# Performance work log

Measured on AMD Instinct MI355X. Metric: run time of the kernel, lower is better.

The kernel has to match this reference:

```python
import jax, jax.numpy as jnp
import numpy as np

KH = KW = 3
STRIDE = 1
PAD = 1
DIL = 1


def _bilinear_gather(data, py, px):
    # data: [B,C,H,W]; py,px: [B,KK,Ho,Wo] absolute sample coords
    B, C, H, W = data.shape
    y0 = jnp.floor(py)
    x0 = jnp.floor(px)
    wy1 = py - y0  # frac weights
    wx1 = px - x0
    wy0 = 1.0 - wy1
    wx0 = 1.0 - wx1
    flat = data.reshape(B, C, H * W)

    def gather(yi, xi):
        valid = (yi >= 0) & (yi < H) & (xi >= 0) & (xi < W)
        yc = jnp.clip(yi, 0, H - 1).astype(jnp.int32)
        xc = jnp.clip(xi, 0, W - 1).astype(jnp.int32)
        idx = yc * W + xc  # [B,KK,Ho,Wo]
        vals = jax.vmap(lambda im, ix: im[:, ix])(flat, idx)  # [B,C,KK,Ho,Wo]
        return vals * valid[:, None].astype(data.dtype)

    out = (gather(y0, x0) * (wy0 * wx0)[:, None]
           + gather(y0, x0 + 1) * (wy0 * wx1)[:, None]
           + gather(y0 + 1, x0) * (wy1 * wx0)[:, None]
           + gather(y0 + 1, x0 + 1) * (wy1 * wx1)[:, None])
    return out  # [B,C,KK,Ho,Wo]


def setup_inputs() -> dict:
    key = jax.random.key(0)
    k1, k2, k3 = jax.random.split(key, 3)
    data = jax.random.normal(k1, (8, 64, 128, 128), dtype=jnp.float32)
    offset = jax.random.normal(k2, (8, 18, 128, 128), dtype=jnp.float32)
    n = 64 * KH * KW
    stdv = 1.0 / np.sqrt(n)
    weight = jax.random.uniform(k3, (64, 64, KH, KW), dtype=jnp.float32,
                                minval=-stdv, maxval=stdv)
    return {"data": data, "offset": offset, "weight": weight}


def reference(data, offset, weight):
    B, C, H, W = data.shape
    Ho = (H + 2 * PAD - (DIL * (KH - 1) + 1)) // STRIDE + 1
    Wo = (W + 2 * PAD - (DIL * (KW - 1) + 1)) // STRIDE + 1
    KK = KH * KW
    # offset layout (deformable_groups=1): [B, 2*KK, Ho, Wo], interleaved (dy, dx) per kernel pt
    off = offset.reshape(B, KK, 2, Ho, Wo)
    off_y = off[:, :, 0]  # [B,KK,Ho,Wo]
    off_x = off[:, :, 1]
    ki = (jnp.arange(KK) // KW).astype(data.dtype)  # kernel row
    kj = (jnp.arange(KK) % KW).astype(data.dtype)   # kernel col
    base_y = (jnp.arange(Ho, dtype=data.dtype) * STRIDE - PAD)[None, :, None] \
             + (ki * DIL)[:, None, None]            # [KK,Ho,1]
    base_x = (jnp.arange(Wo, dtype=data.dtype) * STRIDE - PAD)[None, None, :] \
             + (kj * DIL)[:, None, None]            # [KK,1,Wo]
    py = off_y + base_y[None]  # [B,KK,Ho,Wo]
    px = off_x + base_x[None]
    sampled = _bilinear_gather(data, py, px)  # [B,C,KK,Ho,Wo]
    O = weight.shape[0]
    out = jnp.einsum('bckhw,ock->bohw', sampled, weight.reshape(O, C, KK))
    return out
```

## Files before the change

kernel.cpp:

```cpp
#include <hip/hip_runtime.h>

#define HH 128
#define WW 128
#define CC 64
#define OO 64
#define KK 9
#define PLANE (HH * WW)

#define BAND 11
#define PXB 72
#define BAND_B (BAND * 128 * PXB)
#define POOL_SLOTS 64
#define POOL_OFF BAND_B
#define POOL_B (POOL_SLOTS * 144)
#define DESC_OFF (POOL_OFF + POOL_B)
#define LDS_TOTAL (DESC_OFF + KK * 256 * 16)

typedef _Float16 half8v __attribute__((ext_vector_type(8)));
typedef _Float16 half2v __attribute__((ext_vector_type(2)));
typedef float floatx4 __attribute__((ext_vector_type(4)));

__device__ __forceinline__ unsigned pkpair(float a, float b) {
    return __builtin_bit_cast(unsigned, __builtin_amdgcn_cvt_pkrtz(a, b));
}
__device__ __forceinline__ half2v h2(unsigned u) {
    return __builtin_bit_cast(half2v, u);
}

__global__ __launch_bounds__(256)
void prep_kernel(const float* __restrict__ in, const float* __restrict__ wsrc,
                 unsigned short* __restrict__ outT, _Float16* __restrict__ wt4) {
    __shared__ unsigned tile[64 * 36];
    int blk = blockIdx.x;
    int t = threadIdx.x;
    if (blk < 2048) {
        int b = blk & 7;
        int rest = blk >> 3;
        int y = rest >> 1;
        int xh = rest & 1;
        int p = t & 63;
        int cg = t >> 6;
        const float* src = in + (size_t)(b * 64) * PLANE + y * WW + xh * 64 + p;
#pragma unroll
        for (int i = 0; i < 8; ++i) {
            int c0 = cg * 16 + 2 * i;
            float v0 = src[(size_t)c0 * PLANE];
            float v1 = src[(size_t)(c0 + 1) * PLANE];
            unsigned lo = __builtin_bit_cast(unsigned short, (_Float16)v0);
            unsigned hi = __builtin_bit_cast(unsigned short, (_Float16)v1);
            tile[p * 36 + (c0 >> 1)] = lo | (hi << 16);
        }
        __syncthreads();
        int p2 = t >> 2;
        int q = t & 3;
        const unsigned* s = &tile[p2 * 36 + q * 8];
        uint4 w0 = *(const uint4*)s;
        uint4 w1 = *(const uint4*)(s + 4);
        int half = q >> 1;
        char* dst = (char*)outT + ((size_t)(b * 2 + half) << 20)
                  + (size_t)(y * 128 + xh * 64 + p2) * 64 + (q & 1) * 32;
        *(uint4*)dst = w0;
        *(uint4*)(dst + 16) = w1;
    } else {
        int idx = (blk - 2048) * 256 + t;
        if (idx < 2 * KK * 4 * 64 * 8) {
            int j = idx & 7;
            int lane = (idx >> 3) & 63;
            int nt = (idx >> 9) & 3;
            int pk = idx >> 11;
            int k = pk % 9;
            int pass = pk / 9;
            int o = nt * 16 + (lane & 15);
            int c = pass * 32 + (lane >> 4) * 8 + j;
            wt4[idx] = (_Float16)wsrc[(o * 64 + c) * 9 + k];
        }
    }
}

__global__ __launch_bounds__(1024, 4)
void deform_mfma_kernel(const unsigned short* __restrict__ dataT,
                        const float* __restrict__ offset,
                        const _Float16* __restrict__ wt4,
                        float* __restrict__ out) {
    __shared__ __align__(16) char SB[LDS_TOTAL];
    __shared__ unsigned ovfSrc[POOL_SLOTS];
    __shared__ int ovfCnt;

    const int t = threadIdx.x;
    const int lane = t & 63;
    const int w = t >> 6;
    const int quad = lane >> 4;
    const int l15 = lane & 15;
    const int raw = blockIdx.x;
    const int b = raw & 7;
    const int ho0 = (raw >> 3) * 2;
    const int bs = min(max(ho0 - 4, 0), HH - BAND);

    if (t == 0) ovfCnt = 0;
    __syncthreads();

#pragma unroll
    for (int i = 0; i < 3; ++i) {
        int u = i * 1024 + t;
        if (u < KK * 256) {
            int p = u & 255;
            int k = u >> 8;
            int x = p & 127;
            int ho = ho0 + (p >> 7);
            const float* offp = offset + ((size_t)(b * 18) + 2 * k) * PLANE + ho * WW + x;
            float oy = offp[0];
            float ox = offp[PLANE];
            float py = (float)(ho - 1 + k / 3) + oy;
            float pxx = (float)(x - 1 + k % 3) + ox;
            float y0f = floorf(py);
            float x0f = floorf(pxx);
            float fy = py - y0f;
            float fx = pxx - x0f;
            int y0 = (int)y0f, x0 = (int)x0f;
            int y1 = y0 + 1, x1 = x0 + 1;
            float wy0 = (1.f - fy) * ((y0 >= 0 && y0 < HH) ? 1.f : 0.f);
            float wy1 = fy * ((y1 >= 0 && y1 < HH) ? 1.f : 0.f);
            float wx0 = (1.f - fx) * ((x0 >= 0 && x0 < WW) ? 1.f : 0.f);
            float wx1 = fx * ((x1 >= 0 && x1 < WW) ? 1.f : 0.f);
            int yc0 = min(max(y0, 0), HH - 1);
            int yc1 = min(max(y1, 0), HH - 1);
            int x_lo = min(max(x0, 0), WW - 2);
            float wA = ((x0 == x_lo) ? wx0 : 0.f) + ((x1 == x_lo) ? wx1 : 0.f);
            float wB = ((x0 == x_lo + 1) ? wx0 : 0.f) + ((x1 == x_lo + 1) ? wx1 : 0.f);

            unsigned off0, off1;
            {
                int r = yc0 - bs;
                if (wy0 == 0.f) off0 = (unsigned)(x_lo * PXB);
                else if ((unsigned)r < BAND) off0 = (unsigned)((r * 128 + x_lo) * PXB);
                else {
                    int slot = atomicAdd(&ovfCnt, 1);
                    if (slot < POOL_SLOTS) {
                        ovfSrc[slot] = (unsigned)((yc0 * 128 + x_lo) * 64);
                        off0 = (unsigned)(POOL_OFF + slot * 144);
                    } else {
                        int rc = min(max(r, 0), BAND - 1);
                        off0 = (unsigned)((rc * 128 + x_lo) * PXB);
                    }
                }
            }
            {
                int r = yc1 - bs;
                if (wy1 == 0.f) off1 = (unsigned)(x_lo * PXB);
                else if ((unsigned)r < BAND) off1 = (unsigned)((r * 128 + x_lo) * PXB);
                else {
                    int slot = atomicAdd(&ovfCnt, 1);
                    if (slot < POOL_SLOTS) {
                        ovfSrc[slot] = (unsigned)((yc1 * 128 + x_lo) * 64);
                        off1 = (unsigned)(POOL_OFF + slot * 144);
                    } else {
                        int rc = min(max(r, 0), BAND - 1);
                        off1 = (unsigned)((rc * 128 + x_lo) * PXB);
                    }
                }
            }
            uint4 d;
            d.x = (off0 >> 3) | ((off1 >> 3) << 16);
            d.y = pkpair(wy0 * wA, wy0 * wB);
            d.z = pkpair(wy1 * wA, wy1 * wB);
            d.w = 0;
            *(uint4*)(SB + DESC_OFF + (size_t)(k * 256 + p) * 16) = d;
        }
    }
    __syncthreads();
    const int cnt = min(ovfCnt, POOL_SLOTS);

    floatx4 acc[4];
#pragma unroll
    for (int nt = 0; nt < 4; ++nt)
        acc[nt] = (floatx4){0.f, 0.f, 0.f, 0.f};

    const unsigned qoff = (unsigned)(quad * 16);

    for (int pass = 0; pass < 2; ++pass) {
        if (pass) __syncthreads();
        const char* gh = (const char*)dataT + ((size_t)(b * 2 + pass) << 20);
        {
            const char* gsrc = gh + (unsigned)(bs * 8192);
#pragma unroll
            for (int i = 0; i < 5; ++i) {
                int u = i * 1024 + t;
                uint4 v = *(const uint4*)(gsrc + (size_t)u * 16);
                int pxl = u >> 2, q = u & 3;
                *(uint4*)(SB + pxl * PXB + q * 16) = v;
            }
            if (t < 512) {
                int u = 5120 + t;
                uint4 v = *(const uint4*)(gsrc + (size_t)u * 16);
                int pxl = u >> 2, q = u & 3;
                *(uint4*)(SB + pxl * PXB + q * 16) = v;
            }
            if (t < cnt * 8) {
                int s = t >> 3, j = t & 7, ps = j >> 2, q = j & 3;
                uint4 v = *(const uint4*)(gh + ovfSrc[s] + ps * 64 + q * 16);
                *(uint4*)(SB + POOL_OFF + s * 144 + ps * 72 + q * 16) = v;
            }
        }
        __syncthreads();

        for (int k = 0; k < KK; ++k) {
            uint4 bfr[4];
            const uint4* wk = (const uint4*)wt4 + (size_t)((pass * 9 + k) * 4) * 64 + lane;
#pragma unroll
            for (int nt = 0; nt < 4; ++nt) bfr[nt] = wk[nt * 64];

            int p = w * 16 + l15;
            uint4 d = *(const uint4*)(SB + DESC_OFF + (size_t)(k * 256 + p) * 16);
            unsigned off0 = (d.x & 0xffffu) << 3;
            unsigned off1 = (d.x >> 16) << 3;
            half2v wv0 = h2(d.y), wv1 = h2(d.z);
            half2v h00 = __builtin_shufflevector(wv0, wv0, 0, 0);
            half2v h01 = __builtin_shufflevector(wv0, wv0, 1, 1);
            half2v h10 = __builtin_shufflevector(wv1, wv1, 0, 0);
            half2v h11 = __builtin_shufflevector(wv1, wv1, 1, 1);
            uint4 v00 = *(const uint4*)(SB + off0 + qoff);
            uint4 v01 = *(const uint4*)(SB + off0 + 72 + qoff);
            uint4 v10 = *(const uint4*)(SB + off1 + qoff);
            uint4 v11 = *(const uint4*)(SB + off1 + 72 + qoff);
            half2v s0 = h2(v00.x) * h00 + h2(v01.x) * h01 + h2(v10.x) * h10 + h2(v11.x) * h11;
            half2v s1 = h2(v00.y) * h00 + h2(v01.y) * h01 + h2(v10.y) * h10 + h2(v11.y) * h11;
            half2v s2 = h2(v00.z) * h00 + h2(v01.z) * h01 + h2(v10.z) * h10 + h2(v11.z) * h11;
            half2v s3 = h2(v00.w) * h00 + h2(v01.w) * h01 + h2(v10.w) * h10 + h2(v11.w) * h11;
            uint4 sv = make_uint4(__builtin_bit_cast(unsigned, s0),
                                  __builtin_bit_cast(unsigned, s1),
                                  __builtin_bit_cast(unsigned, s2),
                                  __builtin_bit_cast(unsigned, s3));
            half8v afrag = __builtin_bit_cast(half8v, sv);
#pragma unroll
            for (int nt = 0; nt < 4; ++nt)
                acc[nt] = __builtin_amdgcn_mfma_f32_16x16x32_f16(
                    afrag, __builtin_bit_cast(half8v, bfr[nt]), acc[nt], 0, 0, 0);
        }
    }

#pragma unroll
    for (int nt = 0; nt < 4; ++nt) {
        int o = nt * 16 + l15;
        int p = w * 16 + quad * 4;
        int ho = ho0 + (p >> 7);
        int x = p & 127;
        float* dst = out + (size_t)(b * 64 + o) * PLANE + ho * 128 + x;
        *(floatx4*)dst = acc[nt];
    }
}

__global__ void transpose_weight_kernel(const float* __restrict__ w,
                                        float* __restrict__ wt) {
    int i = blockIdx.x * 256 + threadIdx.x;
    if (i < CC * KK * OO) {
        int o = i & 63;
        int ck = i >> 6;
        wt[i] = w[o * (CC * KK) + ck];
    }
}

__global__ __launch_bounds__(256)
void deform_conv_kernel(const float* __restrict__ data,
                        const float* __restrict__ offset,
                        const float* __restrict__ wt,
                        float* __restrict__ out) {
    const int tid = threadIdx.x;
    const int wo = tid & 127;
    int ohalf = tid >> 7;
    ohalf = __builtin_amdgcn_readfirstlane(ohalf);
    const int row = blockIdx.x;
    const int b = row >> 7;
    const int ho = row & 127;
    int abyte[KK][4];
    float wgt[KK][4];
    const float* offBase = offset + ((size_t)b * 18) * PLANE + ho * WW + wo;
#pragma unroll
    for (int k = 0; k < KK; ++k) {
        float oy = offBase[(2 * k) * PLANE];
        float ox = offBase[(2 * k + 1) * PLANE];
        float py = oy + (float)(ho - 1 + k / 3);
        float px = ox + (float)(wo - 1 + k % 3);
        float y0f = floorf(py);
        float x0f = floorf(px);
        float wy1 = py - y0f, wx1 = px - x0f;
        float wy0 = 1.f - wy1, wx0 = 1.f - wx1;
        int y0 = (int)y0f, x0 = (int)x0f;
        int y1 = y0 + 1, x1 = x0 + 1;
        float my0 = (y0 >= 0 && y0 < HH) ? 1.f : 0.f;
        float my1 = (y1 >= 0 && y1 < HH) ? 1.f : 0.f;
        float mx0 = (x0 >= 0 && x0 < WW) ? 1.f : 0.f;
        float mx1 = (x1 >= 0 && x1 < WW) ? 1.f : 0.f;
        int yc0 = min(max(y0, 0), HH - 1);
        int yc1 = min(max(y1, 0), HH - 1);
        int xc0 = min(max(x0, 0), WW - 1);
        int xc1 = min(max(x1, 0), WW - 1);
        abyte[k][0] = (yc0 * WW + xc0) * 4;
        abyte[k][1] = (yc0 * WW + xc1) * 4;
        abyte[k][2] = (yc1 * WW + xc0) * 4;
        abyte[k][3] = (yc1 * WW + xc1) * 4;
        wgt[k][0] = wy0 * wx0 * my0 * mx0;
        wgt[k][1] = wy0 * wx1 * my0 * mx1;
        wgt[k][2] = wy1 * wx0 * my1 * mx0;
        wgt[k][3] = wy1 * wx1 * my1 * mx1;
    }
    float acc[32];
#pragma unroll
    for (int j = 0; j < 32; ++j) acc[j] = 0.f;
    const float* planeBase = data + (size_t)b * CC * PLANE;
    const float4* wt4base = (const float4*)wt + ohalf * 8;
    for (int c = 0; c < CC; ++c) {
        const char* pc = (const char*)(planeBase + c * PLANE);
#pragma unroll
        for (int k = 0; k < KK; ++k) {
            float v00 = *(const float*)(pc + abyte[k][0]);
            float v01 = *(const float*)(pc + abyte[k][1]);
            float v10 = *(const float*)(pc + abyte[k][2]);
            float v11 = *(const float*)(pc + abyte[k][3]);
            float s = wgt[k][0] * v00 + wgt[k][1] * v01 +
                      wgt[k][2] * v10 + wgt[k][3] * v11;
            const float4* wp = wt4base + (c * KK + k) * 16;
#pragma unroll
            for (int j = 0; j < 8; ++j) {
                float4 wv = wp[j];
                acc[4 * j + 0] += s * wv.x;
                acc[4 * j + 1] += s * wv.y;
                acc[4 * j + 2] += s * wv.z;
                acc[4 * j + 3] += s * wv.w;
            }
        }
    }
    float* outp = out + ((size_t)b * OO + ohalf * 32) * PLANE + ho * WW + wo;
#pragma unroll
    for (int j = 0; j < 32; ++j) outp[j * PLANE] = acc[j];
}

extern "C" void kernel_launch(void* const* d_in, const int* in_sizes, int n_in,
                              void* d_out, int out_size, void* d_ws, size_t ws_size,
                              hipStream_t stream) {
    const float* data = (const float*)d_in[0];
    const float* offset = (const float*)d_in[1];
    const float* weight = (const float*)d_in[2];
    float* out = (float*)d_out;

    const size_t DATA_T_BYTES = (size_t)8 * 2 * 128 * 128 * 64;
    const size_t WT4_BYTES = (size_t)2 * KK * 4 * 64 * 8 * 2;

    if (ws_size >= DATA_T_BYTES + WT4_BYTES) {
        unsigned short* dataT = (unsigned short*)d_ws;
        _Float16* wt4 = (_Float16*)((char*)d_ws + DATA_T_BYTES);
        prep_kernel<<<2048 + 144, 256, 0, stream>>>(data, weight, dataT, wt4);
        deform_mfma_kernel<<<8 * (HH / 2), 1024, 0, stream>>>(dataT, offset, wt4, out);
    } else {
        float* wt = (float*)d_ws;
        int nw = CC * KK * OO;
        transpose_weight_kernel<<<(nw + 255) / 256, 256, 0, stream>>>(weight, wt);
        deform_conv_kernel<<<8 * HH, 256, 0, stream>>>(data, offset, wt, out);
    }
}
```

Baseline: 128.9 us.

## Gather bilinear taps directly from global memory instead of staging LDS band

Removes the per-block staging of an 11-row band of channel-last fp16 data into LDS, along with the overflow pool and its atomics. Bilinear corner values are now read straight from global memory (through L2/L1) using absolute byte offsets stored in the descriptor. Blocks shrink to one output row with 512 threads, and launch bounds become (512, 6) to raise occupancy. This drops the staging loads and the barriers between passes, in exchange for scattered 16-byte global reads that now depend on cache hit rates.

```diff
diff --git a/kernel.cpp b/kernel.cpp
--- a/kernel.cpp
+++ b/kernel.cpp
@@ -7,14 +7,8 @@
 #define KK 9
 #define PLANE (HH * WW)
 
-#define BAND 11
-#define PXB 72
-#define BAND_B (BAND * 128 * PXB)
-#define POOL_SLOTS 64
-#define POOL_OFF BAND_B
-#define POOL_B (POOL_SLOTS * 144)
-#define DESC_OFF (POOL_OFF + POOL_B)
-#define LDS_TOTAL (DESC_OFF + KK * 256 * 16)
+#define DESC_UNITS (KK * 128)
+#define LDS_TOTAL (DESC_UNITS * 16)
 
 typedef _Float16 half8v __attribute__((ext_vector_type(8)));
 typedef _Float16 half2v __attribute__((ext_vector_type(2)));
@@ -77,36 +71,28 @@
     }
 }
 
-__global__ __launch_bounds__(1024, 4)
+__global__ __launch_bounds__(512, 6)
 void deform_mfma_kernel(const unsigned short* __restrict__ dataT,
                         const float* __restrict__ offset,
                         const _Float16* __restrict__ wt4,
                         float* __restrict__ out) {
     __shared__ __align__(16) char SB[LDS_TOTAL];
-    __shared__ unsigned ovfSrc[POOL_SLOTS];
-    __shared__ int ovfCnt;
 
     const int t = threadIdx.x;
     const int lane = t & 63;
     const int w = t >> 6;
-    const int quad = lane >> 4;
+    const unsigned quad = (unsigned)((lane >> 4) & 3);
     const int l15 = lane & 15;
     const int raw = blockIdx.x;
     const int b = raw & 7;
-    const int ho0 = (raw >> 3) * 2;
-    const int bs = min(max(ho0 - 4, 0), HH - BAND);
-
-    if (t == 0) ovfCnt = 0;
-    __syncthreads();
+    const int ho = raw >> 3;
 
 #pragma unroll
     for (int i = 0; i < 3; ++i) {
-        int u = i * 1024 + t;
-        if (u < KK * 256) {
-            int p = u & 255;
-            int k = u >> 8;
-            int x = p & 127;
-            int ho = ho0 + (p >> 7);
+        int u = i * 512 + t;
+        if (u < DESC_UNITS) {
+            int x = u & 127;
+            int k = u >> 7;
             const float* offp = offset + ((size_t)(b * 18) + 2 * k) * PLANE + ho * WW + x;
             float oy = offp[0];
             float ox = offp[PLANE];
@@ -128,100 +114,45 @@
             float wA = ((x0 == x_lo) ? wx0 : 0.f) + ((x1 == x_lo) ? wx1 : 0.f);
             float wB = ((x0 == x_lo + 1) ? wx0 : 0.f) + ((x1 == x_lo + 1) ? wx1 : 0.f);
 
-            unsigned off0, off1;
-            {
-                int r = yc0 - bs;
-                if (wy0 == 0.f) off0 = (unsigned)(x_lo * PXB);
-                else if ((unsigned)r < BAND) off0 = (unsigned)((r * 128 + x_lo) * PXB);
-                else {
-                    int slot = atomicAdd(&ovfCnt, 1);
-                    if (slot < POOL_SLOTS) {
-                        ovfSrc[slot] = (unsigned)((yc0 * 128 + x_lo) * 64);
-                        off0 = (unsigned)(POOL_OFF + slot * 144);
-                    } else {
-                        int rc = min(max(r, 0), BAND - 1);
-                        off0 = (unsigned)((rc * 128 + x_lo) * PXB);
-                    }
-                }
-            }
-            {
-                int r = yc1 - bs;
-                if (wy1 == 0.f) off1 = (unsigned)(x_lo * PXB);
-                else if ((unsigned)r < BAND) off1 = (unsigned)((r * 128 + x_lo) * PXB);
-                else {
-                    int slot = atomicAdd(&ovfCnt, 1);
-                    if (slot < POOL_SLOTS) {
-                        ovfSrc[slot] = (unsigned)((yc1 * 128 + x_lo) * 64);
-                        off1 = (unsigned)(POOL_OFF + slot * 144);
-                    } else {
-                        int rc = min(max(r, 0), BAND - 1);
-                        off1 = (unsigned)((rc * 128 + x_lo) * PXB);
-                    }
-                }
-            }
             uint4 d;
-            d.x = (off0 >> 3) | ((off1 >> 3) << 16);
+            d.x = (unsigned)((yc0 * 128 + x_lo) << 6);
+            d.w = (unsigned)((yc1 * 128 + x_lo) << 6);
             d.y = pkpair(wy0 * wA, wy0 * wB);
             d.z = pkpair(wy1 * wA, wy1 * wB);
-            d.w = 0;
-            *(uint4*)(SB + DESC_OFF + (size_t)(k * 256 + p) * 16) = d;
+            *(uint4*)(SB + (size_t)u * 16) = d;
         }
     }
     __syncthreads();
-    const int cnt = min(ovfCnt, POOL_SLOTS);
 
     floatx4 acc[4];
 #pragma unroll
     for (int nt = 0; nt < 4; ++nt)
         acc[nt] = (floatx4){0.f, 0.f, 0.f, 0.f};
 
-    const unsigned qoff = (unsigned)(quad * 16);
+    const unsigned qoff = quad * 16;
+    const int p = w * 16 + l15;
 
     for (int pass = 0; pass < 2; ++pass) {
-        if (pass) __syncthreads();
         const char* gh = (const char*)dataT + ((size_t)(b * 2 + pass) << 20);
-        {
-            const char* gsrc = gh + (unsigned)(bs * 8192);
-#pragma unroll
-            for (int i = 0; i < 5; ++i) {
-                int u = i * 1024 + t;
-                uint4 v = *(const uint4*)(gsrc + (size_t)u * 16);
-                int pxl = u >> 2, q = u & 3;
-                *(uint4*)(SB + pxl * PXB + q * 16) = v;
-            }
-            if (t < 512) {
-                int u = 5120 + t;
-                uint4 v = *(const uint4*)(gsrc + (size_t)u * 16);
-                int pxl = u >> 2, q = u & 3;
-                *(uint4*)(SB + pxl * PXB + q * 16) = v;
-            }
-            if (t < cnt * 8) {
-                int s = t >> 3, j = t & 7, ps = j >> 2, q = j & 3;
-                uint4 v = *(const uint4*)(gh + ovfSrc[s] + ps * 64 + q * 16);
-                *(uint4*)(SB + POOL_OFF + s * 144 + ps * 72 + q * 16) = v;
-            }
-        }
-        __syncthreads();
-
+#pragma unroll
         for (int k = 0; k < KK; ++k) {
             uint4 bfr[4];
             const uint4* wk = (const uint4*)wt4 + (size_t)((pass * 9 + k) * 4) * 64 + lane;
 #pragma unroll
             for (int nt = 0; nt < 4; ++nt) bfr[nt] = wk[nt * 64];
 
-            int p = w * 16 + l15;
-            uint4 d = *(const uint4*)(SB + DESC_OFF + (size_t)(k * 256 + p) * 16);
-            unsigned off0 = (d.x & 0xffffu) << 3;
-            unsigned off1 = (d.x >> 16) << 3;
+            uint4 d = *(const uint4*)(SB + (size_t)(k * 128 + p) * 16);
             half2v wv0 = h2(d.y), wv1 = h2(d.z);
             half2v h00 = __builtin_shufflevector(wv0, wv0, 0, 0);
             half2v h01 = __builtin_shufflevector(wv0, wv0, 1, 1);
             half2v h10 = __builtin_shufflevector(wv1, wv1, 0, 0);
             half2v h11 = __builtin_shufflevector(wv1, wv1, 1, 1);
-            uint4 v00 = *(const uint4*)(SB + off0 + qoff);
-            uint4 v01 = *(const uint4*)(SB + off0 + 72 + qoff);
-            uint4 v10 = *(const uint4*)(SB + off1 + qoff);
-            uint4 v11 = *(const uint4*)(SB + off1 + 72 + qoff);
+            const char* r0 = gh + d.x + qoff;
+            const char* r1 = gh + d.w + qoff;
+            uint4 v00 = *(const uint4*)r0;
+            uint4 v01 = *(const uint4*)(r0 + 64);
+            uint4 v10 = *(const uint4*)r1;
+            uint4 v11 = *(const uint4*)(r1 + 64);
             half2v s0 = h2(v00.x) * h00 + h2(v01.x) * h01 + h2(v10.x) * h10 + h2(v11.x) * h11;
             half2v s1 = h2(v00.y) * h00 + h2(v01.y) * h01 + h2(v10.y) * h10 + h2(v11.y) * h11;
             half2v s2 = h2(v00.z) * h00 + h2(v01.z) * h01 + h2(v10.z) * h10 + h2(v11.z) * h11;
@@ -241,9 +172,7 @@
 #pragma unroll
     for (int nt = 0; nt < 4; ++nt) {
         int o = nt * 16 + l15;
-        int p = w * 16 + quad * 4;
-        int ho = ho0 + (p >> 7);
-        int x = p & 127;
+        int x = w * 16 + (int)quad * 4;
         float* dst = out + (size_t)(b * 64 + o) * PLANE + ho * 128 + x;
         *(floatx4*)dst = acc[nt];
     }
@@ -349,7 +278,7 @@
         unsigned short* dataT = (unsigned short*)d_ws;
         _Float16* wt4 = (_Float16*)((char*)d_ws + DATA_T_BYTES);
         prep_kernel<<<2048 + 144, 256, 0, stream>>>(data, weight, dataT, wt4);
-        deform_mfma_kernel<<<8 * (HH / 2), 1024, 0, stream>>>(dataT, offset, wt4, out);
+        deform_mfma_kernel<<<8 * HH, 512, 0, stream>>>(dataT, offset, wt4, out);
     } else {
         float* wt = (float*)d_ws;
         int nw = CC * KK * OO;
```

After: 219.3 us. +70.1%, slower.

## Prefetch band data into registers to overlap global loads with descriptor setup

Applied to the files above, without the earlier changes.

Global loads of the pass-0 data band are issued before descriptor computation, and the pass-1 band is loaded into registers before pass-0 compute, so global latency overlaps with other work. Inside each pass the LDS reads for the next kernel point are software-pipelined one iteration ahead. This raises register pressure (about a dozen extra uint4 live across compute) under a 1024-thread launch bound, which may cause spills or lower occupancy.

```diff
diff --git a/kernel.cpp b/kernel.cpp
--- a/kernel.cpp
+++ b/kernel.cpp
@@ -89,7 +89,7 @@
     const int t = threadIdx.x;
     const int lane = t & 63;
     const int w = t >> 6;
-    const int quad = lane >> 4;
+    const unsigned quad = (unsigned)((lane >> 4) & 3);
     const int l15 = lane & 15;
     const int raw = blockIdx.x;
     const int b = raw & 7;
@@ -98,6 +98,16 @@
 
     if (t == 0) ovfCnt = 0;
     __syncthreads();
+
+    const char* gh0 = (const char*)dataT + ((size_t)(b * 2 + 0) << 20);
+    const char* gs0 = gh0 + (unsigned)(bs * 8192);
+    uint4 g0 = *(const uint4*)(gs0 + (size_t)(0 * 1024 + t) * 16);
+    uint4 g1 = *(const uint4*)(gs0 + (size_t)(1 * 1024 + t) * 16);
+    uint4 g2 = *(const uint4*)(gs0 + (size_t)(2 * 1024 + t) * 16);
+    uint4 g3 = *(const uint4*)(gs0 + (size_t)(3 * 1024 + t) * 16);
+    uint4 g4 = *(const uint4*)(gs0 + (size_t)(4 * 1024 + t) * 16);
+    uint4 g5;
+    if (t < 512) g5 = *(const uint4*)(gs0 + (size_t)(5120 + t) * 16);
 
 #pragma unroll
     for (int i = 0; i < 3; ++i) {
@@ -167,65 +177,87 @@
             *(uint4*)(SB + DESC_OFF + (size_t)(k * 256 + p) * 16) = d;
         }
     }
+
+    {
+#pragma unroll
+        for (int i = 0; i < 5; ++i) {
+            unsigned u = (unsigned)(i * 1024 + t);
+            uint4 v = (i == 0) ? g0 : (i == 1) ? g1 : (i == 2) ? g2 : (i == 3) ? g3 : g4;
+            *(uint4*)(SB + (u >> 2) * PXB + (u & 3) * 16) = v;
+        }
+        if (t < 512) {
+            unsigned u = (unsigned)(5120 + t);
+            *(uint4*)(SB + (u >> 2) * PXB + (u & 3) * 16) = g5;
+        }
+    }
     __syncthreads();
     const int cnt = min(ovfCnt, POOL_SLOTS);
 
+    if (cnt > 0) {
+        if (t < cnt * 8) {
+            int s = t >> 3, j = t & 7, ps = j >> 2, q = j & 3;
+            uint4 v = *(const uint4*)(gh0 + ovfSrc[s] + ps * 64 + q * 16);
+            *(uint4*)(SB + POOL_OFF + s * 144 + ps * 72 + q * 16) = v;
+        }
+        __syncthreads();
+    }
+
+    const char* gh1 = (const char*)dataT + ((size_t)(b * 2 + 1) << 20);
+    const char* gs1 = gh1 + (unsigned)(bs * 8192);
+    uint4 h0 = *(const uint4*)(gs1 + (size_t)(0 * 1024 + t) * 16);
+    uint4 h1 = *(const uint4*)(gs1 + (size_t)(1 * 1024 + t) * 16);
+    uint4 h2x = *(const uint4*)(gs1 + (size_t)(2 * 1024 + t) * 16);
+    uint4 h3 = *(const uint4*)(gs1 + (size_t)(3 * 1024 + t) * 16);
+    uint4 h4 = *(const uint4*)(gs1 + (size_t)(4 * 1024 + t) * 16);
+    uint4 h5;
+    if (t < 512) h5 = *(const uint4*)(gs1 + (size_t)(5120 + t) * 16);
+
     floatx4 acc[4];
 #pragma unroll
     for (int nt = 0; nt < 4; ++nt)
         acc[nt] = (floatx4){0.f, 0.f, 0.f, 0.f};
 
-    const unsigned qoff = (unsigned)(quad * 16);
-
-    for (int pass = 0; pass < 2; ++pass) {
-        if (pass) __syncthreads();
-        const char* gh = (const char*)dataT + ((size_t)(b * 2 + pass) << 20);
-        {
-            const char* gsrc = gh + (unsigned)(bs * 8192);
-#pragma unroll
-            for (int i = 0; i < 5; ++i) {
-                int u = i * 1024 + t;
-                uint4 v = *(const uint4*)(gsrc + (size_t)u * 16);
-                int pxl = u >> 2, q = u & 3;
-                *(uint4*)(SB + pxl * PXB + q * 16) = v;
-            }
-            if (t < 512) {
-                int u = 5120 + t;
-                uint4 v = *(const uint4*)(gsrc + (size_t)u * 16);
-                int pxl = u >> 2, q = u & 3;
-                *(uint4*)(SB + pxl * PXB + q * 16) = v;
-            }
-            if (t < cnt * 8) {
-                int s = t >> 3, j = t & 7, ps = j >> 2, q = j & 3;
-                uint4 v = *(const uint4*)(gh + ovfSrc[s] + ps * 64 + q * 16);
-                *(uint4*)(SB + POOL_OFF + s * 144 + ps * 72 + q * 16) = v;
-            }
-        }
-        __syncthreads();
-
+    const unsigned qoff = quad * 16;
+    const int p = w * 16 + l15;
+
+    auto gather_pass = [&](int pass) {
+        uint4 d0 = *(const uint4*)(SB + DESC_OFF + (size_t)(0 * 256 + p) * 16);
+        unsigned off0 = (d0.x & 0xffffu) << 3;
+        unsigned off1 = (d0.x >> 16) << 3;
+        uint4 c00 = *(const uint4*)(SB + off0 + qoff);
+        uint4 c01 = *(const uint4*)(SB + off0 + 72 + qoff);
+        uint4 c10 = *(const uint4*)(SB + off1 + qoff);
+        uint4 c11 = *(const uint4*)(SB + off1 + 72 + qoff);
+        unsigned wy = d0.y, wz = d0.z;
+#pragma unroll
         for (int k = 0; k < KK; ++k) {
             uint4 bfr[4];
             const uint4* wk = (const uint4*)wt4 + (size_t)((pass * 9 + k) * 4) * 64 + lane;
 #pragma unroll
             for (int nt = 0; nt < 4; ++nt) bfr[nt] = wk[nt * 64];
 
-            int p = w * 16 + l15;
-            uint4 d = *(const uint4*)(SB + DESC_OFF + (size_t)(k * 256 + p) * 16);
-            unsigned off0 = (d.x & 0xffffu) << 3;
-            unsigned off1 = (d.x >> 16) << 3;
-            half2v wv0 = h2(d.y), wv1 = h2(d.z);
+            uint4 n00, n01, n10, n11;
+            unsigned nwy, nwz;
+            if (k + 1 < KK) {
+                uint4 dn = *(const uint4*)(SB + DESC_OFF + (size_t)((k + 1) * 256 + p) * 16);
+                unsigned no0 = (dn.x & 0xffffu) << 3;
+                unsigned no1 = (dn.x >> 16) << 3;
+                n00 = *(const uint4*)(SB + no0 + qoff);
+                n01 = *(const uint4*)(SB + no0 + 72 + qoff);
+                n10 = *(const uint4*)(SB + no1 + qoff);
+                n11 = *(const uint4*)(SB + no1 + 72 + qoff);
+                nwy = dn.y; nwz = dn.z;
+            }
+
+            half2v wv0 = h2(wy), wv1 = h2(wz);
             half2v h00 = __builtin_shufflevector(wv0, wv0, 0, 0);
             half2v h01 = __builtin_shufflevector(wv0, wv0, 1, 1);
             half2v h10 = __builtin_shufflevector(wv1, wv1, 0, 0);
             half2v h11 = __builtin_shufflevector(wv1, wv1, 1, 1);
-            uint4 v00 = *(const uint4*)(SB + off0 + qoff);
-            uint4 v01 = *(const uint4*)(SB + off0 + 72 + qoff);
-            uint4 v10 = *(const uint4*)(SB + off1 + qoff);
-            uint4 v11 = *(const uint4*)(SB + off1 + 72 + qoff);
-            half2v s0 = h2(v00.x) * h00 + h2(v01.x) * h01 + h2(v10.x) * h10 + h2(v11.x) * h11;
-            half2v s1 = h2(v00.y) * h00 + h2(v01.y) * h01 + h2(v10.y) * h10 + h2(v11.y) * h11;
-            half2v s2 = h2(v00.z) * h00 + h2(v01.z) * h01 + h2(v10.z) * h10 + h2(v11.z) * h11;
-            half2v s3 = h2(v00.w) * h00 + h2(v01.w) * h01 + h2(v10.w) * h10 + h2(v11.w) * h11;
+            half2v s0 = h2(c00.x) * h00 + h2(c01.x) * h01 + h2(c10.x) * h10 + h2(c11.x) * h11;
+            half2v s1 = h2(c00.y) * h00 + h2(c01.y) * h01 + h2(c10.y) * h10 + h2(c11.y) * h11;
+            half2v s2 = h2(c00.z) * h00 + h2(c01.z) * h01 + h2(c10.z) * h10 + h2(c11.z) * h11;
+            half2v s3 = h2(c00.w) * h00 + h2(c01.w) * h01 + h2(c10.w) * h10 + h2(c11.w) * h11;
             uint4 sv = make_uint4(__builtin_bit_cast(unsigned, s0),
                                   __builtin_bit_cast(unsigned, s1),
                                   __builtin_bit_cast(unsigned, s2),
@@ -235,15 +267,44 @@
             for (int nt = 0; nt < 4; ++nt)
                 acc[nt] = __builtin_amdgcn_mfma_f32_16x16x32_f16(
                     afrag, __builtin_bit_cast(half8v, bfr[nt]), acc[nt], 0, 0, 0);
-        }
-    }
+
+            if (k + 1 < KK) {
+                c00 = n00; c01 = n01; c10 = n10; c11 = n11;
+                wy = nwy; wz = nwz;
+            }
+        }
+    };
+
+    gather_pass(0);
+    __syncthreads();
+
+    {
+#pragma unroll
+        for (int i = 0; i < 5; ++i) {
+            unsigned u = (unsigned)(i * 1024 + t);
+            uint4 v = (i == 0) ? h0 : (i == 1) ? h1 : (i == 2) ? h2x : (i == 3) ? h3 : h4;
+            *(uint4*)(SB + (u >> 2) * PXB + (u & 3) * 16) = v;
+        }
+        if (t < 512) {
+            unsigned u = (unsigned)(5120 + t);
+            *(uint4*)(SB + (u >> 2) * PXB + (u & 3) * 16) = h5;
+        }
+        if (t < cnt * 8) {
+            int s = t >> 3, j = t & 7, ps = j >> 2, q = j & 3;
+            uint4 v = *(const uint4*)(gh1 + ovfSrc[s] + ps * 64 + q * 16);
+            *(uint4*)(SB + POOL_OFF + s * 144 + ps * 72 + q * 16) = v;
+        }
+    }
+    __syncthreads();
+
+    gather_pass(1);
 
 #pragma unroll
     for (int nt = 0; nt < 4; ++nt) {
         int o = nt * 16 + l15;
-        int p = w * 16 + quad * 4;
-        int ho = ho0 + (p >> 7);
-        int x = p & 127;
+        int pp = w * 16 + (int)quad * 4;
+        int ho = ho0 + (pp >> 7);
+        int x = pp & 127;
         float* dst = out + (size_t)(b * 64 + o) * PLANE + ho * 128 + x;
         *(floatx4*)dst = acc[nt];
     }
```

Measured after the change: 129.5 us. Within noise of the previous version (+0.5%).

## Split each row-pair tile into half-width blocks with a 2D LDS data band

Applied to the files above, without the earlier changes.

Each block now covers two output rows by 64 columns with 512 threads instead of two full rows with 1024 threads, so there are twice as many blocks. The staged LDS band becomes a 10-row by 78-column window with a 7-pixel halo, replacing an 11-row full-width band. Samples outside the window fall back to the overflow pool, which is halved to 32 slots. The goal is a smaller LDS footprint per block for better occupancy and load balance, at the cost of redundant halo loads and possibly more overflow fallbacks for large offsets.

```diff
diff --git a/kernel.cpp b/kernel.cpp
--- a/kernel.cpp
+++ b/kernel.cpp
@@ -7,14 +7,15 @@
 #define KK 9
 #define PLANE (HH * WW)
 
-#define BAND 11
+#define XBAND 78
+#define YBAND 10
 #define PXB 72
-#define BAND_B (BAND * 128 * PXB)
-#define POOL_SLOTS 64
+#define BAND_B (YBAND * XBAND * PXB)
+#define POOL_SLOTS 32
 #define POOL_OFF BAND_B
 #define POOL_B (POOL_SLOTS * 144)
 #define DESC_OFF (POOL_OFF + POOL_B)
-#define LDS_TOTAL (DESC_OFF + KK * 256 * 16)
+#define LDS_TOTAL (DESC_OFF + KK * 128 * 16)
 
 typedef _Float16 half8v __attribute__((ext_vector_type(8)));
 typedef _Float16 half2v __attribute__((ext_vector_type(2)));
@@ -77,7 +78,7 @@
     }
 }
 
-__global__ __launch_bounds__(1024, 4)
+__global__ __launch_bounds__(512, 4)
 void deform_mfma_kernel(const unsigned short* __restrict__ dataT,
                         const float* __restrict__ offset,
                         const _Float16* __restrict__ wt4,
@@ -89,24 +90,29 @@
     const int t = threadIdx.x;
     const int lane = t & 63;
     const int w = t >> 6;
-    const int quad = lane >> 4;
+    const unsigned quad = (unsigned)((lane >> 4) & 3);
     const int l15 = lane & 15;
     const int raw = blockIdx.x;
     const int b = raw & 7;
-    const int ho0 = (raw >> 3) * 2;
-    const int bs = min(max(ho0 - 4, 0), HH - BAND);
+    const int rest = raw >> 3;
+    const int xh = rest & 1;
+    const int ho0 = (rest >> 1) * 2;
+    const int cx0 = xh * 64;
+    const int bs = min(max(ho0 - 4, 0), HH - YBAND);
 
     if (t == 0) ovfCnt = 0;
     __syncthreads();
 
+    int cnt = 0;
+
 #pragma unroll
     for (int i = 0; i < 3; ++i) {
-        int u = i * 1024 + t;
-        if (u < KK * 256) {
-            int p = u & 255;
-            int k = u >> 8;
-            int x = p & 127;
-            int ho = ho0 + (p >> 7);
+        int u = i * 512 + t;
+        if (u < KK * 128) {
+            int p = u & 127;
+            int k = u >> 7;
+            int x = cx0 + (p & 63);
+            int ho = ho0 + (p >> 6);
             const float* offp = offset + ((size_t)(b * 18) + 2 * k) * PLANE + ho * WW + x;
             float oy = offp[0];
             float ox = offp[PLANE];
@@ -128,34 +134,40 @@
             float wA = ((x0 == x_lo) ? wx0 : 0.f) + ((x1 == x_lo) ? wx1 : 0.f);
             float wB = ((x0 == x_lo + 1) ? wx0 : 0.f) + ((x1 == x_lo + 1) ? wx1 : 0.f);
 
+            int s_lo = x_lo - cx0 + 7;
+            int s_safe = min(max(s_lo, 0), XBAND - 2);
+            bool col_ok = (s_lo >= 0) && (s_lo <= XBAND - 2);
+
             unsigned off0, off1;
             {
                 int r = yc0 - bs;
-                if (wy0 == 0.f) off0 = (unsigned)(x_lo * PXB);
-                else if ((unsigned)r < BAND) off0 = (unsigned)((r * 128 + x_lo) * PXB);
+                if (wy0 == 0.f) off0 = (unsigned)(s_safe * PXB);
+                else if ((unsigned)r < YBAND && col_ok)
+                    off0 = (unsigned)((r * XBAND + s_lo) * PXB);
                 else {
                     int slot = atomicAdd(&ovfCnt, 1);
                     if (slot < POOL_SLOTS) {
                         ovfSrc[slot] = (unsigned)((yc0 * 128 + x_lo) * 64);
                         off0 = (unsigned)(POOL_OFF + slot * 144);
                     } else {
-                        int rc = min(max(r, 0), BAND - 1);
-                        off0 = (unsigned)((rc * 128 + x_lo) * PXB);
+                        int rc = min(max(r, 0), YBAND - 1);
+                        off0 = (unsigned)((rc * XBAND + s_safe) * PXB);
                     }
                 }
             }
             {
                 int r = yc1 - bs;
-                if (wy1 == 0.f) off1 = (unsigned)(x_lo * PXB);
-                else if ((unsigned)r < BAND) off1 = (unsigned)((r * 128 + x_lo) * PXB);
+                if (wy1 == 0.f) off1 = (unsigned)(s_safe * PXB);
+                else if ((unsigned)r < YBAND && col_ok)
+                    off1 = (unsigned)((r * XBAND + s_lo) * PXB);
                 else {
                     int slot = atomicAdd(&ovfCnt, 1);
                     if (slot < POOL_SLOTS) {
                         ovfSrc[slot] = (unsigned)((yc1 * 128 + x_lo) * 64);
                         off1 = (unsigned)(POOL_OFF + slot * 144);
                     } else {
-                        int rc = min(max(r, 0), BAND - 1);
-                        off1 = (unsigned)((rc * 128 + x_lo) * PXB);
+                        int rc = min(max(r, 0), YBAND - 1);
+                        off1 = (unsigned)((rc * XBAND + s_safe) * PXB);
                     }
                 }
             }
@@ -164,53 +176,56 @@
             d.y = pkpair(wy0 * wA, wy0 * wB);
             d.z = pkpair(wy1 * wA, wy1 * wB);
             d.w = 0;
-            *(uint4*)(SB + DESC_OFF + (size_t)(k * 256 + p) * 16) = d;
-        }
-    }
-    __syncthreads();
-    const int cnt = min(ovfCnt, POOL_SLOTS);
+            *(uint4*)(SB + DESC_OFF + (size_t)(k * 128 + p) * 16) = d;
+        }
+    }
+
+    auto stage_band = [&](const char* gh) {
+#pragma unroll
+        for (int i = 0; i < 6; ++i) {
+            int u = i * 512 + t;
+            int px = u >> 2, q = u & 3;
+            int r = px / XBAND;
+            int c = px - r * XBAND;
+            int gcol = min(max(cx0 - 7 + c, 0), 127);
+            uint4 v = *(const uint4*)(gh + (size_t)(((bs + r) * 128 + gcol) * 64) + q * 16);
+            *(uint4*)(SB + (size_t)(px * PXB) + q * 16) = v;
+        }
+        if (t < 48) {
+            int u = 3072 + t;
+            int px = u >> 2, q = u & 3;
+            int r = px / XBAND;
+            int c = px - r * XBAND;
+            int gcol = min(max(cx0 - 7 + c, 0), 127);
+            uint4 v = *(const uint4*)(gh + (size_t)(((bs + r) * 128 + gcol) * 64) + q * 16);
+            *(uint4*)(SB + (size_t)(px * PXB) + q * 16) = v;
+        }
+    };
+    auto pool_stage = [&](const char* gh) {
+        if (t < cnt * 8) {
+            int s = t >> 3, j = t & 7, ps = j >> 2, q = j & 3;
+            uint4 v = *(const uint4*)(gh + ovfSrc[s] + ps * 64 + q * 16);
+            *(uint4*)(SB + POOL_OFF + s * 144 + ps * 72 + q * 16) = v;
+        }
+    };
 
     floatx4 acc[4];
 #pragma unroll
     for (int nt = 0; nt < 4; ++nt)
         acc[nt] = (floatx4){0.f, 0.f, 0.f, 0.f};
 
-    const unsigned qoff = (unsigned)(quad * 16);
-
-    for (int pass = 0; pass < 2; ++pass) {
-        if (pass) __syncthreads();
-        const char* gh = (const char*)dataT + ((size_t)(b * 2 + pass) << 20);
-        {
-            const char* gsrc = gh + (unsigned)(bs * 8192);
-#pragma unroll
-            for (int i = 0; i < 5; ++i) {
-                int u = i * 1024 + t;
-                uint4 v = *(const uint4*)(gsrc + (size_t)u * 16);
-                int pxl = u >> 2, q = u & 3;
-                *(uint4*)(SB + pxl * PXB + q * 16) = v;
-            }
-            if (t < 512) {
-                int u = 5120 + t;
-                uint4 v = *(const uint4*)(gsrc + (size_t)u * 16);
-                int pxl = u >> 2, q = u & 3;
-                *(uint4*)(SB + pxl * PXB + q * 16) = v;
-            }
-            if (t < cnt * 8) {
-                int s = t >> 3, j = t & 7, ps = j >> 2, q = j & 3;
-                uint4 v = *(const uint4*)(gh + ovfSrc[s] + ps * 64 + q * 16);
-                *(uint4*)(SB + POOL_OFF + s * 144 + ps * 72 + q * 16) = v;
-            }
-        }
-        __syncthreads();
-
+    const unsigned qoff = quad * 16;
+    const int p = w * 16 + l15;
+
+    auto gather = [&](int pass) {
+#pragma unroll
         for (int k = 0; k < KK; ++k) {
             uint4 bfr[4];
             const uint4* wk = (const uint4*)wt4 + (size_t)((pass * 9 + k) * 4) * 64 + lane;
 #pragma unroll
             for (int nt = 0; nt < 4; ++nt) bfr[nt] = wk[nt * 64];
 
-            int p = w * 16 + l15;
-            uint4 d = *(const uint4*)(SB + DESC_OFF + (size_t)(k * 256 + p) * 16);
+            uint4 d = *(const uint4*)(SB + DESC_OFF + (size_t)(k * 128 + p) * 16);
             unsigned off0 = (d.x & 0xffffu) << 3;
             unsigned off1 = (d.x >> 16) << 3;
             half2v wv0 = h2(d.y), wv1 = h2(d.z);
@@ -236,14 +251,29 @@
                 acc[nt] = __builtin_amdgcn_mfma_f32_16x16x32_f16(
                     afrag, __builtin_bit_cast(half8v, bfr[nt]), acc[nt], 0, 0, 0);
         }
-    }
+    };
+
+    const char* gh0 = (const char*)dataT + ((size_t)(b * 2 + 0) << 20);
+    const char* gh1 = (const char*)dataT + ((size_t)(b * 2 + 1) << 20);
+
+    stage_band(gh0);
+    __syncthreads();
+    cnt = min(ovfCnt, POOL_SLOTS);
+    pool_stage(gh0);
+    __syncthreads();
+    gather(0);
+    __syncthreads();
+    stage_band(gh1);
+    pool_stage(gh1);
+    __syncthreads();
+    gather(1);
 
 #pragma unroll
     for (int nt = 0; nt < 4; ++nt) {
         int o = nt * 16 + l15;
-        int p = w * 16 + quad * 4;
-        int ho = ho0 + (p >> 7);
-        int x = p & 127;
+        int pp = w * 16 + (int)quad * 4;
+        int ho = ho0 + (pp >> 6);
+        int x = cx0 + (pp & 63);
         float* dst = out + (size_t)(b * 64 + o) * PLANE + ho * 128 + x;
         *(floatx4*)dst = acc[nt];
     }
@@ -349,7 +379,7 @@
         unsigned short* dataT = (unsigned short*)d_ws;
         _Float16* wt4 = (_Float16*)((char*)d_ws + DATA_T_BYTES);
         prep_kernel<<<2048 + 144, 256, 0, stream>>>(data, weight, dataT, wt4);
-        deform_mfma_kernel<<<8 * (HH / 2), 1024, 0, stream>>>(dataT, offset, wt4, out);
+        deform_mfma_kernel<<<8 * HH, 512, 0, stream>>>(dataT, offset, wt4, out);
     } else {
         float* wt = (float*)d_ws;
         int nw = CC * KK * OO;
```

Measured after the change: 128.8 us. Within noise of the previous version (-0.1%).
